# Kernel optimization log

Hardware: AMD Instinct MI355X
Metric: run time of the kernel (lower is better)

## Reference

```python
import jax, jax.numpy as jnp
import numpy as np
from jax import lax

L, H, NUM_CONVS, KSIZE = 8192, 128, 4, 7
EPS = 1e-5


def _pos_encoding(length, dim, dtype):
    pos = jnp.arange(length, dtype=jnp.float32)[:, None]
    i = jnp.arange(dim, dtype=jnp.float32)[None, :]
    angle = pos / jnp.power(10000.0, (2.0 * jnp.floor(i / 2.0)) / dim)
    pe = jnp.where((jnp.arange(dim) % 2 == 0)[None, :], jnp.sin(angle), jnp.cos(angle))
    return pe.astype(dtype)


def _layer_norm(x):
    mu = jnp.mean(x, axis=-1, keepdims=True)
    var = jnp.mean(jnp.square(x - mu), axis=-1, keepdims=True)
    return (x - mu) * lax.rsqrt(var + EPS)


def _conv1d_same(x, w, b):
    # x: [L, H]; w: [H_out, H_in, K]; b: [H_out]. SAME padding over sequence.
    lhs = x.T[None]  # [1, H, L]
    out = lax.conv_general_dilated(lhs, w, window_strides=(1,), padding='SAME',
                                   dimension_numbers=('NCH', 'OIH', 'NCH'))
    return (out[0] + b[:, None]).T  # [L, H]


def setup_inputs() -> dict:
    key = jax.random.key(0)
    ks = jax.random.split(key, 12)
    s = 0.02
    return {
        'x': jax.random.normal(ks[0], (L, H), jnp.float32),
        'conv_w': jax.random.normal(ks[1], (NUM_CONVS, H, H, KSIZE), jnp.float32) * s,
        'conv_b': jax.random.normal(ks[2], (NUM_CONVS, H), jnp.float32) * s,
        'Wq': jax.random.normal(ks[3], (H, H), jnp.float32) * s,
        'bq': jax.random.normal(ks[4], (H,), jnp.float32) * s,
        'Wk': jax.random.normal(ks[5], (H, H), jnp.float32) * s,
        'bk': jax.random.normal(ks[6], (H,), jnp.float32) * s,
        'Wv': jax.random.normal(ks[7], (H, H), jnp.float32) * s,
        'bv': jax.random.normal(ks[8], (H,), jnp.float32) * s,
        'Wff': jax.random.normal(ks[9], (H, H), jnp.float32) * s,
        'bff': jax.random.normal(ks[10], (H,), jnp.float32) * s,
    }


def reference(x, conv_w, conv_b, Wq, bq, Wk, bk, Wv, bv, Wff, bff):
    h = x + _pos_encoding(x.shape[0], x.shape[1], x.dtype)
    # conv stack: LN -> conv -> residual, repeated num_convs times
    for i in range(NUM_CONVS):
        residual = h
        h = _conv1d_same(_layer_norm(h), conv_w[i], conv_b[i]) + residual
    # self-attention (single-head as written in the source)
    residual = h
    n = _layer_norm(h)
    q = n @ Wq.T + bq
    k = n @ Wk.T + bk
    v = n @ Wv.T + bv
    scale = 1.0 / jnp.sqrt(jnp.asarray(H, h.dtype))
    attn = jax.nn.softmax((q @ k.T) * scale, axis=-1)  # [L, L]
    h = attn @ v + residual
    # feed-forward
    residual = h
    h = jax.nn.relu(_layer_norm(h) @ Wff.T + bff) + residual
    return h
```

## Files before the change

kernel.cpp:

```cpp
#include <hip/hip_runtime.h>

#define LL 8192
#define HH 128

typedef __attribute__((ext_vector_type(8))) short short8v;
typedef __attribute__((ext_vector_type(4))) short short4v;
typedef __attribute__((ext_vector_type(4))) float f32x4;
typedef __attribute__((ext_vector_type(16))) float f32x16;

__device__ inline short f2bf(float f) {
    union { float f; unsigned u; } x; x.f = f;
    unsigned r = (x.u + 0x7fffu + ((x.u >> 16) & 1u)) >> 16;
    return (short)r;
}
__device__ inline float bf2f(short s) {
    union { unsigned u; float f; } x; x.u = ((unsigned)(unsigned short)s) << 16;
    return x.f;
}

__device__ inline float fexp2(float x) {
#if defined(__has_builtin)
#if __has_builtin(__builtin_amdgcn_exp2f)
    return __builtin_amdgcn_exp2f(x);
#else
    return __expf(x * 0.6931471805599453f);
#endif
#else
    return __expf(x * 0.6931471805599453f);
#endif
}

__device__ inline unsigned pack_hi16(unsigned hi, unsigned lo) {
#if defined(__has_builtin)
#if __has_builtin(__builtin_amdgcn_perm)
    return __builtin_amdgcn_perm(hi, lo, 0x07060302u);
#endif
#endif
    return (lo >> 16) | (hi & 0xffff0000u);
}

__device__ inline void plane32swap(unsigned& a, unsigned& b) {
#if defined(__has_builtin)
#if __has_builtin(__builtin_amdgcn_permlane32_swap)
    typedef unsigned u2v __attribute__((ext_vector_type(2)));
    u2v r = __builtin_amdgcn_permlane32_swap(a, b, false, false);
    a = r[0]; b = r[1];
    return;
#endif
#endif
    asm volatile("v_permlane32_swap_b32 %0, %1" : "+v"(a), "+v"(b));
}

__device__ inline short* sAp(short* base, int row, int col) {
    int byte = (row << 8) + (col << 1);
    byte ^= (row & 7) << 4;
    return (short*)((char*)base + byte);
}

__device__ inline short8v ln_pack8(const float* rowF, int l15) {
    const float4 a = *(const float4*)&rowF[l15 * 8];
    const float4 b = *(const float4*)&rowF[l15 * 8 + 4];
    float s  = (a.x + a.y) + (a.z + a.w) + (b.x + b.y) + (b.z + b.w);
    float s2 = a.x * a.x + a.y * a.y + a.z * a.z + a.w * a.w
             + b.x * b.x + b.y * b.y + b.z * b.z + b.w * b.w;
#pragma unroll
    for (int off = 1; off <= 8; off <<= 1) {
        s  += __shfl_xor(s,  off, 64);
        s2 += __shfl_xor(s2, off, 64);
    }
    float mu = s * (1.f / 128.f);
    float var = s2 * (1.f / 128.f) - mu * mu;
    float rstd = rsqrtf(var + 1e-5f);
    short8v r;
    r[0] = f2bf((a.x - mu) * rstd);
    r[1] = f2bf((a.y - mu) * rstd);
    r[2] = f2bf((a.z - mu) * rstd);
    r[3] = f2bf((a.w - mu) * rstd);
    r[4] = f2bf((b.x - mu) * rstd);
    r[5] = f2bf((b.y - mu) * rstd);
    r[6] = f2bf((b.z - mu) * rstd);
    r[7] = f2bf((b.w - mu) * rstd);
    return r;
}

__global__ __launch_bounds__(256) void repack_all(const float* __restrict__ w,
                                                  const float* __restrict__ Wq,
                                                  const float* __restrict__ Wk,
                                                  const float* __restrict__ Wv,
                                                  const float* __restrict__ bq,
                                                  const float* __restrict__ bk,
                                                  const float* __restrict__ bv,
                                                  const float* __restrict__ Wff,
                                                  short* __restrict__ wkb,
                                                  short* __restrict__ wqkvb,
                                                  float* __restrict__ b3,
                                                  short* __restrict__ wffb) {
    const float qs = 0.08838834764831845f * 1.4426950408889634f;
    int idx = blockIdx.x * 256 + threadIdx.x;
    if (idx < 458752) {
        int i = idx & (HH - 1);
        int t = idx >> 7;
        int o = t & (HH - 1);
        int t2 = t >> 7;
        int k = t2 % 7;
        int lay = t2 / 7;
        wkb[idx] = f2bf(w[((lay * HH + o) * HH + i) * 7 + k]);
    } else {
        int j = idx - 458752;
        if (j < 49152) {
            int t = j >> 14, r = j & 16383;
            float v = (t == 0) ? Wq[r] * qs : (t == 1) ? Wk[r] : Wv[r];
            wqkvb[j] = f2bf(v);
        } else if (j < 49536) {
            int jj = j - 49152;
            b3[jj] = (jj < 128) ? bq[jj] * qs : (jj < 256) ? bk[jj - 128] : bv[jj - 256];
        } else if (j < 65920) {
            int jj = j - 49536;
            wffb[jj] = f2bf(Wff[jj]);
        }
    }
}

__global__ __launch_bounds__(256, 2) void conv4_qkv_kernel(const float* __restrict__ x,
                                                           const short* __restrict__ wkb,
                                                           const float* __restrict__ conv_b,
                                                           const short* __restrict__ wqkvb,
                                                           const float* __restrict__ b3,
                                                           float* __restrict__ hB,
                                                           short* __restrict__ qb,
                                                           short* __restrict__ kb,
                                                           short* __restrict__ vt) {
    __shared__ float sF[40][132];
    __shared__ short sA[54 * 128];
    __shared__ short sT[4][32][17];
    int tid = threadIdx.x;
    int w = tid >> 6, lane = tid & 63;
    int l15 = lane & 15, quad = lane >> 4;
    int wg = blockIdx.x;
    int m0 = ((wg & 7) * 64 + (wg >> 3)) * 16;
    int c0 = w * 32;

    for (int idx = tid; idx < 40 * 32; idx += 256) {
        int r = idx >> 5, c4 = (idx & 31) << 2;
        int g = m0 - 12 + r;
        float4 val = make_float4(0.f, 0.f, 0.f, 0.f);
        if (g >= 0 && g < LL) {
            val = *(const float4*)&x[g * HH + c4];
            float fg = (float)g;
#pragma unroll
            for (int h = 0; h < 2; h++) {
                int i0 = c4 + h * 2;
                float e = (float)i0 / 128.f;
                float rev = fg * fexp2(e * -13.287712379549449f - 2.651496129472319f);
                rev -= floorf(rev);
                float ang = rev * 6.283185307179586f;
                ((float*)&val)[h * 2]     += __sinf(ang);
                ((float*)&val)[h * 2 + 1] += __cosf(ang);
            }
        }
        *(float4*)&sF[r][c4] = val;
    }
    __syncthreads();
#pragma unroll
    for (int rr = 0; rr < 3; rr++) {
        int row = rr * 16 + w * 4 + quad;
        if (row < 40)
            *(short8v*)sAp(sA, row, l15 * 8) = ln_pack8(&sF[row][0], l15);
    }
    __syncthreads();

    const float* cb = conv_b;

    {
        const short* wl = wkb + 0 * 7 * HH * HH;
        f32x4 a0a = (f32x4)(0.f), a0b = (f32x4)(0.f);
        f32x4 a1a = (f32x4)(0.f), a1b = (f32x4)(0.f);
        f32x4 a2a = (f32x4)(0.f), a2b = (f32x4)(0.f);
#pragma unroll
        for (int k = 0; k < 7; k++) {
            const short* bw0 = wl + (k * HH + c0 + l15) * HH;
            const short* bw1 = bw0 + 16 * HH;
#pragma unroll
            for (int ks = 0; ks < 4; ks++) {
                short8v bf0 = *(const short8v*)&bw0[ks * 32 + quad * 8];
                short8v bf1 = *(const short8v*)&bw1[ks * 32 + quad * 8];
                short8v af0 = *(const short8v*)sAp(sA,      l15 + k, ks * 32 + quad * 8);
                short8v af1 = *(const short8v*)sAp(sA, 16 + l15 + k, ks * 32 + quad * 8);
                short8v af2 = *(const short8v*)sAp(sA, 32 + l15 + k, ks * 32 + quad * 8);
                a0a = __builtin_amdgcn_mfma_f32_16x16x32_bf16(af0, bf0, a0a, 0, 0, 0);
                a0b = __builtin_amdgcn_mfma_f32_16x16x32_bf16(af0, bf1, a0b, 0, 0, 0);
                a1a = __builtin_amdgcn_mfma_f32_16x16x32_bf16(af1, bf0, a1a, 0, 0, 0);
                a1b = __builtin_amdgcn_mfma_f32_16x16x32_bf16(af1, bf1, a1b, 0, 0, 0);
                a2a = __builtin_amdgcn_mfma_f32_16x16x32_bf16(af2, bf0, a2a, 0, 0, 0);
                a2b = __builtin_amdgcn_mfma_f32_16x16x32_bf16(af2, bf1, a2b, 0, 0, 0);
            }
        }
        float bl = cb[0 * HH + c0 + l15], bh = cb[0 * HH + c0 + 16 + l15];
#pragma unroll
        for (int r = 0; r < 4; r++) {
            int rr0 = quad * 4 + r;
            sF[3 + rr0][c0 + l15]       += a0a[r] + bl;
            sF[3 + rr0][c0 + 16 + l15]  += a0b[r] + bh;
            sF[19 + rr0][c0 + l15]      += a1a[r] + bl;
            sF[19 + rr0][c0 + 16 + l15] += a1b[r] + bh;
            if (rr0 < 2) {
                sF[35 + rr0][c0 + l15]      += a2a[r] + bl;
                sF[35 + rr0][c0 + 16 + l15] += a2b[r] + bh;
            }
        }
    }
    __syncthreads();
#pragma unroll
    for (int rr = 0; rr < 3; rr++) {
        int row = 3 + rr * 16 + w * 4 + quad;
        if (row < 37) {
            short8v pk = ln_pack8(&sF[row][0], l15);
            int g = m0 - 12 + row;
            if (g < 0 || g >= LL) pk = (short8v)(short)0;
            *(short8v*)sAp(sA, row, l15 * 8) = pk;
        }
    }
    __syncthreads();

    {
        const short* wl = wkb + 1 * 7 * HH * HH;
        f32x4 a0a = (f32x4)(0.f), a0b = (f32x4)(0.f);
        f32x4 a1a = (f32x4)(0.f), a1b = (f32x4)(0.f);
#pragma unroll
        for (int k = 0; k < 7; k++) {
            const short* bw0 = wl + (k * HH + c0 + l15) * HH;
            const short* bw1 = bw0 + 16 * HH;
#pragma unroll
            for (int ks = 0; ks < 4; ks++) {
                short8v bf0 = *(const short8v*)&bw0[ks * 32 + quad * 8];
                short8v bf1 = *(const short8v*)&bw1[ks * 32 + quad * 8];
                short8v af0 = *(const short8v*)sAp(sA,  3 + l15 + k, ks * 32 + quad * 8);
                short8v af1 = *(const short8v*)sAp(sA, 19 + l15 + k, ks * 32 + quad * 8);
                a0a = __builtin_amdgcn_mfma_f32_16x16x32_bf16(af0, bf0, a0a, 0, 0, 0);
                a0b = __builtin_amdgcn_mfma_f32_16x16x32_bf16(af0, bf1, a0b, 0, 0, 0);
                a1a = __builtin_amdgcn_mfma_f32_16x16x32_bf16(af1, bf0, a1a, 0, 0, 0);
                a1b = __builtin_amdgcn_mfma_f32_16x16x32_bf16(af1, bf1, a1b, 0, 0, 0);
            }
        }
        float bl = cb[1 * HH + c0 + l15], bh = cb[1 * HH + c0 + 16 + l15];
#pragma unroll
        for (int r = 0; r < 4; r++) {
            int rr0 = quad * 4 + r;
            sF[6 + rr0][c0 + l15]      += a0a[r] + bl;
            sF[6 + rr0][c0 + 16 + l15] += a0b[r] + bh;
            if (rr0 < 12) {
                sF[22 + rr0][c0 + l15]      += a1a[r] + bl;
                sF[22 + rr0][c0 + 16 + l15] += a1b[r] + bh;
            }
        }
    }
    __syncthreads();
#pragma unroll
    for (int rr = 0; rr < 2; rr++) {
        int row = 6 + rr * 16 + w * 4 + quad;
        if (row < 34) {
            short8v pk = ln_pack8(&sF[row][0], l15);
            int g = m0 - 12 + row;
            if (g < 0 || g >= LL) pk = (short8v)(short)0;
            *(short8v*)sAp(sA, row, l15 * 8) = pk;
        }
    }
    __syncthreads();

    {
        const short* wl = wkb + 2 * 7 * HH * HH;
        f32x4 a0a = (f32x4)(0.f), a0b = (f32x4)(0.f);
        f32x4 a1a = (f32x4)(0.f), a1b = (f32x4)(0.f);
#pragma unroll
        for (int k = 0; k < 7; k++) {
            const short* bw0 = wl + (k * HH + c0 + l15) * HH;
            const short* bw1 = bw0 + 16 * HH;
#pragma unroll
            for (int ks = 0; ks < 4; ks++) {
                short8v bf0 = *(const short8v*)&bw0[ks * 32 + quad * 8];
                short8v bf1 = *(const short8v*)&bw1[ks * 32 + quad * 8];
                short8v af0 = *(const short8v*)sAp(sA,  6 + l15 + k, ks * 32 + quad * 8);
                short8v af1 = *(const short8v*)sAp(sA, 22 + l15 + k, ks * 32 + quad * 8);
                a0a = __builtin_amdgcn_mfma_f32_16x16x32_bf16(af0, bf0, a0a, 0, 0, 0);
                a0b = __builtin_amdgcn_mfma_f32_16x16x32_bf16(af0, bf1, a0b, 0, 0, 0);
                a1a = __builtin_amdgcn_mfma_f32_16x16x32_bf16(af1, bf0, a1a, 0, 0, 0);
                a1b = __builtin_amdgcn_mfma_f32_16x16x32_bf16(af1, bf1, a1b, 0, 0, 0);
            }
        }
        float bl = cb[2 * HH + c0 + l15], bh = cb[2 * HH + c0 + 16 + l15];
#pragma unroll
        for (int r = 0; r < 4; r++) {
            int rr0 = quad * 4 + r;
            sF[9 + rr0][c0 + l15]      += a0a[r] + bl;
            sF[9 + rr0][c0 + 16 + l15] += a0b[r] + bh;
            if (rr0 < 6) {
                sF[25 + rr0][c0 + l15]      += a1a[r] + bl;
                sF[25 + rr0][c0 + 16 + l15] += a1b[r] + bh;
            }
        }
    }
    __syncthreads();
#pragma unroll
    for (int rr = 0; rr < 2; rr++) {
        int row = 9 + rr * 16 + w * 4 + quad;
        if (row < 31) {
            short8v pk = ln_pack8(&sF[row][0], l15);
            int g = m0 - 12 + row;
            if (g < 0 || g >= LL) pk = (short8v)(short)0;
            *(short8v*)sAp(sA, row, l15 * 8) = pk;
        }
    }
    __syncthreads();

    {
        const short* wl = wkb + 3 * 7 * HH * HH;
        f32x4 a0a = (f32x4)(0.f), a0b = (f32x4)(0.f);
#pragma unroll
        for (int k = 0; k < 7; k++) {
            const short* bw0 = wl + (k * HH + c0 + l15) * HH;
            const short* bw1 = bw0 + 16 * HH;
#pragma unroll
            for (int ks = 0; ks < 4; ks++) {
                short8v bf0 = *(const short8v*)&bw0[ks * 32 + quad * 8];
                short8v bf1 = *(const short8v*)&bw1[ks * 32 + quad * 8];
                short8v af = *(const short8v*)sAp(sA, 9 + l15 + k, ks * 32 + quad * 8);
                a0a = __builtin_amdgcn_mfma_f32_16x16x32_bf16(af, bf0, a0a, 0, 0, 0);
                a0b = __builtin_amdgcn_mfma_f32_16x16x32_bf16(af, bf1, a0b, 0, 0, 0);
            }
        }
        float bl = cb[3 * HH + c0 + l15], bh = cb[3 * HH + c0 + 16 + l15];
#pragma unroll
        for (int r = 0; r < 4; r++) {
            int rr0 = quad * 4 + r;
            int g = m0 + rr0;
            float v0 = sF[12 + rr0][c0 + l15]      + a0a[r] + bl;
            float v1 = sF[12 + rr0][c0 + 16 + l15] + a0b[r] + bh;
            sF[12 + rr0][c0 + l15]      = v0;
            sF[12 + rr0][c0 + 16 + l15] = v1;
            hB[g * HH + c0 + l15]      = v0;
            hB[g * HH + c0 + 16 + l15] = v1;
        }
    }
    __syncthreads();
    {
        int row = w * 4 + quad;
        *(short8v*)sAp(sA, row, l15 * 8) = ln_pack8(&sF[12 + row][0], l15);
    }
    __syncthreads();
    short8v af4[4];
#pragma unroll
    for (int ks = 0; ks < 4; ks++)
        af4[ks] = *(const short8v*)sAp(sA, l15, ks * 32 + quad * 8);

#pragma unroll
    for (int t = 0; t < 3; t++) {
        f32x4 acc0 = (f32x4)(0.f), acc1 = (f32x4)(0.f);
        const short* b0 = wqkvb + (t * 128 + c0 + l15) * HH;
        const short* b1 = b0 + 16 * HH;
#pragma unroll
        for (int ks = 0; ks < 4; ks++) {
            short8v bf0 = *(const short8v*)&b0[ks * 32 + quad * 8];
            short8v bf1 = *(const short8v*)&b1[ks * 32 + quad * 8];
            acc0 = __builtin_amdgcn_mfma_f32_16x16x32_bf16(af4[ks], bf0, acc0, 0, 0, 0);
            acc1 = __builtin_amdgcn_mfma_f32_16x16x32_bf16(af4[ks], bf1, acc1, 0, 0, 0);
        }
        float qb0 = b3[t * 128 + c0 + l15], qb1 = b3[t * 128 + c0 + 16 + l15];
        if (t < 2) {
            short* o = (t == 0) ? qb : kb;
#pragma unroll
            for (int r = 0; r < 4; r++) {
                int lr = m0 + quad * 4 + r;
                o[lr * HH + c0 + l15]      = f2bf(acc0[r] + qb0);
                o[lr * HH + c0 + 16 + l15] = f2bf(acc1[r] + qb1);
            }
        } else {
#pragma unroll
            for (int r = 0; r < 4; r++) {
                sT[w][l15][quad * 4 + r]      = f2bf(acc0[r] + qb0);
                sT[w][16 + l15][quad * 4 + r] = f2bf(acc1[r] + qb1);
            }
            asm volatile("s_waitcnt lgkmcnt(0)" ::: "memory");
#pragma unroll
            for (int cc = 0; cc < 8; cc++) {
                int col = cc * 4 + quad;
                vt[(c0 + col) * LL + m0 + l15] = sT[w][col][l15];
            }
        }
    }
}

#define FBN 64
#define NSPLIT 8
#define SEGROWS (LL / NSPLIT)

__global__ __launch_bounds__(256, 2) void flash_mfma_kernel(const short* __restrict__ qs,
                                                            const short* __restrict__ ksrc,
                                                            const short* __restrict__ vsrc,
                                                            short* __restrict__ PO,
                                                            float* __restrict__ Pl) {
    __shared__ short sK[16 * 64 * 8];
    __shared__ short sV[16 * 64 * 8];

    const int tid = threadIdx.x;
    const int w = tid >> 6, lane = tid & 63;
    const int l31 = lane & 31, hi = lane >> 5;
    const int seg = blockIdx.x & 7;
    const int m0 = (blockIdx.x >> 3) * 128;
    const int jbeg = seg * SEGROWS;
    const int nchunk = SEGROWS >> 6;
    const int qrow = m0 + w * 32 + l31;

    short8v qf[8];
#pragma unroll
    for (int ks = 0; ks < 8; ks++)
        qf[ks] = *(const short8v*)&qs[qrow * HH + ks * 16 + hi * 8];

    float l_r = 0.f;
    f32x16 o_acc[4];
#pragma unroll
    for (int dt = 0; dt < 4; dt++) o_acc[dt] = (f32x16)(0.f);

    short8v kr[4], vr[4];
#pragma unroll
    for (int r = 0; r < 4; r++) {
        int s = w + 4 * r;
        kr[r] = *(const short8v*)&ksrc[(jbeg + (s >> 3) * 32 + l31) * HH + (s & 7) * 16 + hi * 8];
        vr[r] = *(const short8v*)&vsrc[((s >> 2) * 32 + l31) * LL + jbeg + (s & 3) * 16 + hi * 8];
    }

    for (int c = 0; c < nchunk; c++) {
        __syncthreads();
#pragma unroll
        for (int r = 0; r < 4; r++) {
            int s = w + 4 * r;
            *(short8v*)&sK[(s * 64 + lane) * 8] = kr[r];
            *(short8v*)&sV[(s * 64 + lane) * 8] = vr[r];
        }
        __syncthreads();
        if (c + 1 < nchunk) {
            const int j1 = jbeg + (c + 1) * FBN;
#pragma unroll
            for (int r = 0; r < 4; r++) {
                int s = w + 4 * r;
                kr[r] = *(const short8v*)&ksrc[(j1 + (s >> 3) * 32 + l31) * HH + (s & 7) * 16 + hi * 8];
                vr[r] = *(const short8v*)&vsrc[((s >> 2) * 32 + l31) * LL + j1 + (s & 3) * 16 + hi * 8];
            }
        }
        f32x16 s0 = (f32x16)(0.f), s1 = (f32x16)(0.f);
        __builtin_amdgcn_s_setprio(1);
#pragma unroll
        for (int ks = 0; ks < 8; ks++) {
            short8v kf0 = *(const short8v*)&sK[((ks) * 64 + lane) * 8];
            short8v kf1 = *(const short8v*)&sK[((8 + ks) * 64 + lane) * 8];
            s0 = __builtin_amdgcn_mfma_f32_32x32x16_bf16(kf0, qf[ks], s0, 0, 0, 0);
            s1 = __builtin_amdgcn_mfma_f32_32x32x16_bf16(kf1, qf[ks], s1, 0, 0, 0);
        }
        __builtin_amdgcn_s_setprio(0);
        short8v pfrag[4];
#pragma unroll
        for (int nt = 0; nt < 2; nt++) {
            const f32x16& sa = nt ? s1 : s0;
            unsigned pw[8];
#pragma unroll
            for (int m = 0; m < 8; m++) {
                float p0 = fexp2(sa[2 * m]);
                float p1 = fexp2(sa[2 * m + 1]);
                l_r += p0 + p1;
                union { float f; unsigned u; } u0, u1;
                u0.f = p0; u1.f = p1;
                pw[m] = pack_hi16(u1.u, u0.u);
            }
            plane32swap(pw[0], pw[2]);
            plane32swap(pw[1], pw[3]);
            plane32swap(pw[4], pw[6]);
            plane32swap(pw[5], pw[7]);
            union { unsigned u[4]; short8v v; } fa, fb;
            fa.u[0] = pw[0]; fa.u[1] = pw[1]; fa.u[2] = pw[2]; fa.u[3] = pw[3];
            fb.u[0] = pw[4]; fb.u[1] = pw[5]; fb.u[2] = pw[6]; fb.u[3] = pw[7];
            pfrag[nt * 2]     = fa.v;
            pfrag[nt * 2 + 1] = fb.v;
        }
        __builtin_amdgcn_s_setprio(1);
#pragma unroll
        for (int ks = 0; ks < 4; ks++)
#pragma unroll
            for (int dt = 0; dt < 4; dt++) {
                short8v vf = *(const short8v*)&sV[((dt * 4 + ks) * 64 + lane) * 8];
                o_acc[dt] = __builtin_amdgcn_mfma_f32_32x32x16_bf16(pfrag[ks], vf, o_acc[dt], 0, 0, 0);
            }
        __builtin_amdgcn_s_setprio(0);
    }
    float lsum = l_r + __shfl_xor(l_r, 32, 64);
    if (hi == 0)
        Pl[seg * LL + qrow] = lsum;
#pragma unroll
    for (int dt = 0; dt < 4; dt++)
#pragma unroll
        for (int i = 0; i < 16; i++) {
            int qr = (i & 3) + 8 * (i >> 2) + 4 * hi;
            PO[(size_t)seg * LL * HH + (size_t)(m0 + w * 32 + qr) * HH + dt * 32 + l31] =
                f2bf(o_acc[dt][i]);
        }
}

__global__ __launch_bounds__(256) void ff_kernel(const float* __restrict__ hin,
                                                 const short* __restrict__ PO,
                                                 const float* __restrict__ Pl,
                                                 const short* __restrict__ wffb,
                                                 const float* __restrict__ bff,
                                                 float* __restrict__ out) {
    __shared__ float sF[16][132];
    __shared__ short sA[16 * 128];
    int tid = threadIdx.x;
    int w = tid >> 6, lane = tid & 63;
    int l15 = lane & 15, quad = lane >> 4;
    int wg = blockIdx.x;
    int m0 = ((wg & 7) * 64 + (wg >> 3)) * 16;
    int row = w * 4 + quad;
    int grow = m0 + row;

    float s = 0.f;
#pragma unroll
    for (int seg = 0; seg < NSPLIT; seg++) s += Pl[seg * LL + grow];
    float li = 1.f / s;

    float acc[8] = {0.f, 0.f, 0.f, 0.f, 0.f, 0.f, 0.f, 0.f};
#pragma unroll
    for (int seg = 0; seg < NSPLIT; seg++) {
        short8v pv = *(const short8v*)&PO[(size_t)seg * LL * HH + (size_t)grow * HH + l15 * 8];
#pragma unroll
        for (int j = 0; j < 8; j++) acc[j] += bf2f(pv[j]);
    }
    float4 h0v = *(const float4*)&hin[grow * HH + l15 * 8];
    float4 h1v = *(const float4*)&hin[grow * HH + l15 * 8 + 4];
    float m[8];
    m[0] = h0v.x + acc[0] * li; m[1] = h0v.y + acc[1] * li;
    m[2] = h0v.z + acc[2] * li; m[3] = h0v.w + acc[3] * li;
    m[4] = h1v.x + acc[4] * li; m[5] = h1v.y + acc[5] * li;
    m[6] = h1v.z + acc[6] * li; m[7] = h1v.w + acc[7] * li;
    *(float4*)&sF[row][l15 * 8]     = make_float4(m[0], m[1], m[2], m[3]);
    *(float4*)&sF[row][l15 * 8 + 4] = make_float4(m[4], m[5], m[6], m[7]);
    {
        float ss  = (m[0] + m[1]) + (m[2] + m[3]) + (m[4] + m[5]) + (m[6] + m[7]);
        float ss2 = m[0]*m[0] + m[1]*m[1] + m[2]*m[2] + m[3]*m[3]
                  + m[4]*m[4] + m[5]*m[5] + m[6]*m[6] + m[7]*m[7];
#pragma unroll
        for (int off = 1; off <= 8; off <<= 1) {
            ss  += __shfl_xor(ss,  off, 64);
            ss2 += __shfl_xor(ss2, off, 64);
        }
        float mu = ss * (1.f / 128.f);
        float var = ss2 * (1.f / 128.f) - mu * mu;
        float rstd = rsqrtf(var + 1e-5f);
        short8v r;
#pragma unroll
        for (int j = 0; j < 8; j++) r[j] = f2bf((m[j] - mu) * rstd);
        *(short8v*)sAp(sA, row, l15 * 8) = r;
    }
    __syncthreads();
    int c0 = w * 32;
    f32x4 acc0 = (f32x4)(0.f), acc1 = (f32x4)(0.f);
    const short* b0 = wffb + (c0 + l15) * HH;
    const short* b1 = b0 + 16 * HH;
#pragma unroll
    for (int ks = 0; ks < 4; ks++) {
        short8v af = *(const short8v*)sAp(sA, l15, ks * 32 + quad * 8);
        short8v bf0 = *(const short8v*)&b0[ks * 32 + quad * 8];
        short8v bf1 = *(const short8v*)&b1[ks * 32 + quad * 8];
        acc0 = __builtin_amdgcn_mfma_f32_16x16x32_bf16(af, bf0, acc0, 0, 0, 0);
        acc1 = __builtin_amdgcn_mfma_f32_16x16x32_bf16(af, bf1, acc1, 0, 0, 0);
    }
    float bb0 = bff[c0 + l15], bb1 = bff[c0 + 16 + l15];
#pragma unroll
    for (int r = 0; r < 4; r++) {
        int lr = quad * 4 + r;
        out[(m0 + lr) * HH + c0 + l15]      = fmaxf(acc0[r] + bb0, 0.f) + sF[lr][c0 + l15];
        out[(m0 + lr) * HH + c0 + 16 + l15] = fmaxf(acc1[r] + bb1, 0.f) + sF[lr][c0 + 16 + l15];
    }
}

extern "C" void kernel_launch(void* const* d_in, const int* in_sizes, int n_in,
                              void* d_out, int out_size, void* d_ws, size_t ws_size,
                              hipStream_t stream) {
    const float* x      = (const float*)d_in[0];
    const float* conv_w = (const float*)d_in[1];
    const float* conv_b = (const float*)d_in[2];
    const float* Wq = (const float*)d_in[3];
    const float* bq = (const float*)d_in[4];
    const float* Wk = (const float*)d_in[5];
    const float* bk = (const float*)d_in[6];
    const float* Wv = (const float*)d_in[7];
    const float* bv = (const float*)d_in[8];
    const float* Wff = (const float*)d_in[9];
    const float* bff = (const float*)d_in[10];
    float* out = (float*)d_out;

    char* ws = (char*)d_ws;
    const size_t MB = 1u << 20;
    float* hB   = (float*)(ws);
    short* qb   = (short*)(ws + 4 * MB);
    short* kb   = (short*)(ws + 6 * MB);
    short* vt   = (short*)(ws + 8 * MB);
    float* Pl   = (float*)(ws + 10 * MB);
    short* wffb = (short*)(ws + 10 * MB + 524288);
    short* PO   = (short*)(ws + 10 * MB + 524288 + 32768);
    short* wkb   = (short*)(ws + 16 * MB);
    short* wqkvb = (short*)(ws + 17 * MB);
    float* b3    = (float*)(ws + 17 * MB + 131072);

    repack_all<<<2050, 256, 0, stream>>>(conv_w, Wq, Wk, Wv, bq, bk, bv, Wff,
                                         wkb, wqkvb, b3, wffb);
    conv4_qkv_kernel<<<LL / 16, 256, 0, stream>>>(x, wkb, conv_b, wqkvb, b3,
                                                  hB, qb, kb, vt);
    flash_mfma_kernel<<<LL / 128 * NSPLIT, 256, 0, stream>>>(qb, kb, vt, PO, Pl);
    ff_kernel<<<LL / 16, 256, 0, stream>>>(hB, PO, Pl, wffb, bff, out);
}
```

Baseline: 191.1 us.

## Stream conv weights through LDS with async global_load_lds prefetch pipeline

After: 191.5 us. About the same (+0.2%).

```diff
diff --git a/kernel.cpp b/kernel.cpp
--- a/kernel.cpp
+++ b/kernel.cpp
@@ -133,12 +133,26 @@
     __shared__ float sF[40][132];
     __shared__ short sA[54 * 128];
     __shared__ short sT[4][32][17];
+    __shared__ short wbuf[16 * 1024];
     int tid = threadIdx.x;
     int w = tid >> 6, lane = tid & 63;
     int l15 = lane & 15, quad = lane >> 4;
     int wg = blockIdx.x;
     int m0 = ((wg & 7) * 64 + (wg >> 3)) * 16;
     int c0 = w * 32;
+
+#define WISSUE(wl_, s_)                                                          \
+    {                                                                            \
+        int k_ = (s_) >> 2, ks_ = (s_) & 3;                                      \
+        const short* g0_ = (wl_) + (k_ * HH + c0 + l15) * HH + ks_ * 32 + quad * 8; \
+        short* l0_ = &wbuf[(((s_) & 3) * 4 + w) * 1024];                         \
+        __builtin_amdgcn_global_load_lds(                                        \
+            (const __attribute__((address_space(1))) void*)g0_,                  \
+            (__attribute__((address_space(3))) void*)l0_, 16, 0, 0);             \
+        __builtin_amdgcn_global_load_lds(                                        \
+            (const __attribute__((address_space(1))) void*)(g0_ + 16 * HH),      \
+            (__attribute__((address_space(3))) void*)(l0_ + 512), 16, 0, 0);     \
+    }
 
     for (int idx = tid; idx < 40 * 32; idx += 256) {
         int r = idx >> 5, c4 = (idx & 31) << 2;
@@ -176,24 +190,25 @@
         f32x4 a0a = (f32x4)(0.f), a0b = (f32x4)(0.f);
         f32x4 a1a = (f32x4)(0.f), a1b = (f32x4)(0.f);
         f32x4 a2a = (f32x4)(0.f), a2b = (f32x4)(0.f);
-#pragma unroll
-        for (int k = 0; k < 7; k++) {
-            const short* bw0 = wl + (k * HH + c0 + l15) * HH;
-            const short* bw1 = bw0 + 16 * HH;
-#pragma unroll
-            for (int ks = 0; ks < 4; ks++) {
-                short8v bf0 = *(const short8v*)&bw0[ks * 32 + quad * 8];
-                short8v bf1 = *(const short8v*)&bw1[ks * 32 + quad * 8];
-                short8v af0 = *(const short8v*)sAp(sA,      l15 + k, ks * 32 + quad * 8);
-                short8v af1 = *(const short8v*)sAp(sA, 16 + l15 + k, ks * 32 + quad * 8);
-                short8v af2 = *(const short8v*)sAp(sA, 32 + l15 + k, ks * 32 + quad * 8);
-                a0a = __builtin_amdgcn_mfma_f32_16x16x32_bf16(af0, bf0, a0a, 0, 0, 0);
-                a0b = __builtin_amdgcn_mfma_f32_16x16x32_bf16(af0, bf1, a0b, 0, 0, 0);
-                a1a = __builtin_amdgcn_mfma_f32_16x16x32_bf16(af1, bf0, a1a, 0, 0, 0);
-                a1b = __builtin_amdgcn_mfma_f32_16x16x32_bf16(af1, bf1, a1b, 0, 0, 0);
-                a2a = __builtin_amdgcn_mfma_f32_16x16x32_bf16(af2, bf0, a2a, 0, 0, 0);
-                a2b = __builtin_amdgcn_mfma_f32_16x16x32_bf16(af2, bf1, a2b, 0, 0, 0);
-            }
+        WISSUE(wl, 0); WISSUE(wl, 1); WISSUE(wl, 2);
+#pragma unroll
+        for (int s = 0; s < 28; s++) {
+            if (s + 3 < 28) WISSUE(wl, s + 3);
+            const int rem = 27 - s;
+            const int nf = (rem < 3 ? rem : 3) * 2;
+            asm volatile("s_waitcnt vmcnt(%0)" :: "n"(nf) : "memory");
+            int k = s >> 2, ks = s & 3;
+            short8v bf0 = *(const short8v*)&wbuf[((s & 3) * 4 + w) * 1024 + lane * 8];
+            short8v bf1 = *(const short8v*)&wbuf[((s & 3) * 4 + w) * 1024 + 512 + lane * 8];
+            short8v af0 = *(const short8v*)sAp(sA,      l15 + k, ks * 32 + quad * 8);
+            short8v af1 = *(const short8v*)sAp(sA, 16 + l15 + k, ks * 32 + quad * 8);
+            short8v af2 = *(const short8v*)sAp(sA, 32 + l15 + k, ks * 32 + quad * 8);
+            a0a = __builtin_amdgcn_mfma_f32_16x16x32_bf16(af0, bf0, a0a, 0, 0, 0);
+            a0b = __builtin_amdgcn_mfma_f32_16x16x32_bf16(af0, bf1, a0b, 0, 0, 0);
+            a1a = __builtin_amdgcn_mfma_f32_16x16x32_bf16(af1, bf0, a1a, 0, 0, 0);
+            a1b = __builtin_amdgcn_mfma_f32_16x16x32_bf16(af1, bf1, a1b, 0, 0, 0);
+            a2a = __builtin_amdgcn_mfma_f32_16x16x32_bf16(af2, bf0, a2a, 0, 0, 0);
+            a2b = __builtin_amdgcn_mfma_f32_16x16x32_bf16(af2, bf1, a2b, 0, 0, 0);
         }
         float bl = cb[0 * HH + c0 + l15], bh = cb[0 * HH + c0 + 16 + l15];
 #pragma unroll
@@ -226,21 +241,22 @@
         const short* wl = wkb + 1 * 7 * HH * HH;
         f32x4 a0a = (f32x4)(0.f), a0b = (f32x4)(0.f);
         f32x4 a1a = (f32x4)(0.f), a1b = (f32x4)(0.f);
-#pragma unroll
-        for (int k = 0; k < 7; k++) {
-            const short* bw0 = wl + (k * HH + c0 + l15) * HH;
-            const short* bw1 = bw0 + 16 * HH;
-#pragma unroll
-            for (int ks = 0; ks < 4; ks++) {
-                short8v bf0 = *(const short8v*)&bw0[ks * 32 + quad * 8];
-                short8v bf1 = *(const short8v*)&bw1[ks * 32 + quad * 8];
-                short8v af0 = *(const short8v*)sAp(sA,  3 + l15 + k, ks * 32 + quad * 8);
-                short8v af1 = *(const short8v*)sAp(sA, 19 + l15 + k, ks * 32 + quad * 8);
-                a0a = __builtin_amdgcn_mfma_f32_16x16x32_bf16(af0, bf0, a0a, 0, 0, 0);
-                a0b = __builtin_amdgcn_mfma_f32_16x16x32_bf16(af0, bf1, a0b, 0, 0, 0);
-                a1a = __builtin_amdgcn_mfma_f32_16x16x32_bf16(af1, bf0, a1a, 0, 0, 0);
-                a1b = __builtin_amdgcn_mfma_f32_16x16x32_bf16(af1, bf1, a1b, 0, 0, 0);
-            }
+        WISSUE(wl, 0); WISSUE(wl, 1); WISSUE(wl, 2);
+#pragma unroll
+        for (int s = 0; s < 28; s++) {
+            if (s + 3 < 28) WISSUE(wl, s + 3);
+            const int rem = 27 - s;
+            const int nf = (rem < 3 ? rem : 3) * 2;
+            asm volatile("s_waitcnt vmcnt(%0)" :: "n"(nf) : "memory");
+            int k = s >> 2, ks = s & 3;
+            short8v bf0 = *(const short8v*)&wbuf[((s & 3) * 4 + w) * 1024 + lane * 8];
+            short8v bf1 = *(const short8v*)&wbuf[((s & 3) * 4 + w) * 1024 + 512 + lane * 8];
+            short8v af0 = *(const short8v*)sAp(sA,  3 + l15 + k, ks * 32 + quad * 8);
+            short8v af1 = *(const short8v*)sAp(sA, 19 + l15 + k, ks * 32 + quad * 8);
+            a0a = __builtin_amdgcn_mfma_f32_16x16x32_bf16(af0, bf0, a0a, 0, 0, 0);
+            a0b = __builtin_amdgcn_mfma_f32_16x16x32_bf16(af0, bf1, a0b, 0, 0, 0);
+            a1a = __builtin_amdgcn_mfma_f32_16x16x32_bf16(af1, bf0, a1a, 0, 0, 0);
+            a1b = __builtin_amdgcn_mfma_f32_16x16x32_bf16(af1, bf1, a1b, 0, 0, 0);
         }
         float bl = cb[1 * HH + c0 + l15], bh = cb[1 * HH + c0 + 16 + l15];
 #pragma unroll
@@ -271,21 +287,22 @@
         const short* wl = wkb + 2 * 7 * HH * HH;
         f32x4 a0a = (f32x4)(0.f), a0b = (f32x4)(0.f);
         f32x4 a1a = (f32x4)(0.f), a1b = (f32x4)(0.f);
-#pragma unroll
-        for (int k = 0; k < 7; k++) {
-            const short* bw0 = wl + (k * HH + c0 + l15) * HH;
-            const short* bw1 = bw0 + 16 * HH;
-#pragma unroll
-            for (int ks = 0; ks < 4; ks++) {
-                short8v bf0 = *(const short8v*)&bw0[ks * 32 + quad * 8];
-                short8v bf1 = *(const short8v*)&bw1[ks * 32 + quad * 8];
-                short8v af0 = *(const short8v*)sAp(sA,  6 + l15 + k, ks * 32 + quad * 8);
-                short8v af1 = *(const short8v*)sAp(sA, 22 + l15 + k, ks * 32 + quad * 8);
-                a0a = __builtin_amdgcn_mfma_f32_16x16x32_bf16(af0, bf0, a0a, 0, 0, 0);
-                a0b = __builtin_amdgcn_mfma_f32_16x16x32_bf16(af0, bf1, a0b, 0, 0, 0);
-                a1a = __builtin_amdgcn_mfma_f32_16x16x32_bf16(af1, bf0, a1a, 0, 0, 0);
-                a1b = __builtin_amdgcn_mfma_f32_16x16x32_bf16(af1, bf1, a1b, 0, 0, 0);
-            }
+        WISSUE(wl, 0); WISSUE(wl, 1); WISSUE(wl, 2);
+#pragma unroll
+        for (int s = 0; s < 28; s++) {
+            if (s + 3 < 28) WISSUE(wl, s + 3);
+            const int rem = 27 - s;
+            const int nf = (rem < 3 ? rem : 3) * 2;
+            asm volatile("s_waitcnt vmcnt(%0)" :: "n"(nf) : "memory");
+            int k = s >> 2, ks = s & 3;
+            short8v bf0 = *(const short8v*)&wbuf[((s & 3) * 4 + w) * 1024 + lane * 8];
+            short8v bf1 = *(const short8v*)&wbuf[((s & 3) * 4 + w) * 1024 + 512 + lane * 8];
+            short8v af0 = *(const short8v*)sAp(sA,  6 + l15 + k, ks * 32 + quad * 8);
+            short8v af1 = *(const short8v*)sAp(sA, 22 + l15 + k, ks * 32 + quad * 8);
+            a0a = __builtin_amdgcn_mfma_f32_16x16x32_bf16(af0, bf0, a0a, 0, 0, 0);
+            a0b = __builtin_amdgcn_mfma_f32_16x16x32_bf16(af0, bf1, a0b, 0, 0, 0);
+            a1a = __builtin_amdgcn_mfma_f32_16x16x32_bf16(af1, bf0, a1a, 0, 0, 0);
+            a1b = __builtin_amdgcn_mfma_f32_16x16x32_bf16(af1, bf1, a1b, 0, 0, 0);
         }
         float bl = cb[2 * HH + c0 + l15], bh = cb[2 * HH + c0 + 16 + l15];
 #pragma unroll
@@ -315,18 +332,19 @@
     {
         const short* wl = wkb + 3 * 7 * HH * HH;
         f32x4 a0a = (f32x4)(0.f), a0b = (f32x4)(0.f);
-#pragma unroll
-        for (int k = 0; k < 7; k++) {
-            const short* bw0 = wl + (k * HH + c0 + l15) * HH;
-            const short* bw1 = bw0 + 16 * HH;
-#pragma unroll
-            for (int ks = 0; ks < 4; ks++) {
-                short8v bf0 = *(const short8v*)&bw0[ks * 32 + quad * 8];
-                short8v bf1 = *(const short8v*)&bw1[ks * 32 + quad * 8];
-                short8v af = *(const short8v*)sAp(sA, 9 + l15 + k, ks * 32 + quad * 8);
-                a0a = __builtin_amdgcn_mfma_f32_16x16x32_bf16(af, bf0, a0a, 0, 0, 0);
-                a0b = __builtin_amdgcn_mfma_f32_16x16x32_bf16(af, bf1, a0b, 0, 0, 0);
-            }
+        WISSUE(wl, 0); WISSUE(wl, 1); WISSUE(wl, 2);
+#pragma unroll
+        for (int s = 0; s < 28; s++) {
+            if (s + 3 < 28) WISSUE(wl, s + 3);
+            const int rem = 27 - s;
+            const int nf = (rem < 3 ? rem : 3) * 2;
+            asm volatile("s_waitcnt vmcnt(%0)" :: "n"(nf) : "memory");
+            int k = s >> 2, ks = s & 3;
+            short8v bf0 = *(const short8v*)&wbuf[((s & 3) * 4 + w) * 1024 + lane * 8];
+            short8v bf1 = *(const short8v*)&wbuf[((s & 3) * 4 + w) * 1024 + 512 + lane * 8];
+            short8v af = *(const short8v*)sAp(sA, 9 + l15 + k, ks * 32 + quad * 8);
+            a0a = __builtin_amdgcn_mfma_f32_16x16x32_bf16(af, bf0, a0a, 0, 0, 0);
+            a0b = __builtin_amdgcn_mfma_f32_16x16x32_bf16(af, bf1, a0b, 0, 0, 0);
         }
         float bl = cb[3 * HH + c0 + l15], bh = cb[3 * HH + c0 + 16 + l15];
 #pragma unroll
@@ -387,6 +405,7 @@
             }
         }
     }
+#undef WISSUE
 }
 
 #define FBN 64
```
